# Kernel optimization log

Measured on AMD Instinct MI355X. Metric: run time of the kernel, lower is better.

Reference implementation:

```python
import jax, jax.numpy as jnp
import numpy as np

N, E, G, L = 50000, 800000, 256, 3
D, NF, EF, OUT = 300, 128, 16, 128
BN_EPS = 1e-5


def setup_inputs() -> dict:
    key = jax.random.key(0)
    ks = jax.random.split(key, 24)
    s = 0.02
    inp = {
        "node_feat": jax.random.normal(ks[0], (N, NF), jnp.float32),
        "edge_feat": jax.random.normal(ks[1], (E, EF), jnp.float32),
        "src": jax.random.randint(ks[2], (E,), 0, N),
        "dst": jax.random.randint(ks[3], (E,), 0, N),
        "graph_ids": jnp.sort(jax.random.randint(ks[4], (N,), 0, G)),
        "num_graphs": G,
        # encoder params
        "node_W": jax.random.normal(ks[5], (NF, D), jnp.float32) * s,
        "node_b": jnp.zeros((D,), jnp.float32),
        # per-layer edge encoders [L, EF, D]
        "edge_W": jax.random.normal(ks[6], (L, EF, D), jnp.float32) * s,
        "edge_b": jnp.zeros((L, D), jnp.float32),
        # per-layer GINEConv MLP: Linear(D,2D) BN ReLU Linear(2D,D) BN
        "W1": jax.random.normal(ks[7], (L, D, 2 * D), jnp.float32) * s,
        "b1": jnp.zeros((L, 2 * D), jnp.float32),
        "g1": jnp.ones((L, 2 * D), jnp.float32),
        "beta1": jnp.zeros((L, 2 * D), jnp.float32),
        "W2": jax.random.normal(ks[8], (L, 2 * D, D), jnp.float32) * s,
        "b2": jnp.zeros((L, D), jnp.float32),
        "g2": jnp.ones((L, D), jnp.float32),
        "beta2": jnp.zeros((L, D), jnp.float32),
        # prediction head
        "pred_W": jax.random.normal(ks[9], (D, OUT), jnp.float32) * s,
        "pred_b": jnp.zeros((OUT,), jnp.float32),
    }
    return inp


def _bn(x, g, b):
    # BatchNorm1d in training mode: biased batch statistics
    m = jnp.mean(x, axis=0)
    v = jnp.var(x, axis=0)
    return (x - m) * jax.lax.rsqrt(v + BN_EPS) * g + b


def reference(node_feat, edge_feat, src, dst, graph_ids, num_graphs,
              node_W, node_b, edge_W, edge_b,
              W1, b1, g1, beta1, W2, b2, g2, beta2,
              pred_W, pred_b):
    n_nodes = node_feat.shape[0]
    n_layers = edge_W.shape[0]
    hn = node_feat @ node_W + node_b  # [N, D]
    for l in range(n_layers):
        he = edge_feat @ edge_W[l] + edge_b[l]            # [E, D]
        msg = jax.nn.relu(hn[src] + he)                   # gather + edge fuse
        agg = jax.ops.segment_sum(msg, dst, num_segments=n_nodes)
        h = hn + agg                                      # (1+eps)*h + agg, eps=0
        h = jax.nn.relu(_bn(h @ W1[l] + b1[l], g1[l], beta1[l]))
        h = _bn(h @ W2[l] + b2[l], g2[l], beta2[l])
        hn = jax.nn.relu(h) if l != n_layers - 1 else h   # dropout p=0 -> identity
    # AvgPooling over nodes per graph
    cnt = jax.ops.segment_sum(jnp.ones((n_nodes, 1), hn.dtype), graph_ids,
                              num_segments=num_graphs)
    hg = jax.ops.segment_sum(hn, graph_ids, num_segments=num_graphs)
    hg = hg / jnp.maximum(cnt, 1.0)
    return hg @ pred_W + pred_b  # [G, OUT]
```

## Files before the change

### kernel.cpp

```cpp
#include <hip/hip_runtime.h>

#define N_NODES 50000
#define N_EDGES 800000
#define N_GRAPHS 256
#define N_LAYERS 3
#define DIM 300
#define NFEAT 128
#define EFEAT 16
#define OUTD 128
#define BN_EPS 1e-5f

typedef __attribute__((ext_vector_type(8))) short bfrag8;
typedef __attribute__((ext_vector_type(4))) float facc4;
typedef __attribute__((ext_vector_type(4))) unsigned short us4;
typedef __attribute__((ext_vector_type(8))) unsigned short us8;

__device__ __forceinline__ unsigned short f2bf(float f) {
    unsigned u = __float_as_uint(f);
    unsigned r = ((u >> 16) & 1u) + 0x7fffu;
    return (unsigned short)((u + r) >> 16);
}
__device__ __forceinline__ float bf2f(unsigned short h) {
    return __uint_as_float(((unsigned)h) << 16);
}
__device__ __forceinline__ void split2(float v, unsigned short& h, unsigned short& l) {
    h = f2bf(v);
    l = f2bf(v - bf2f(h));
}

__device__ __forceinline__ void load_lds16(const void* gsrc, void* ldsdst) {
    __builtin_amdgcn_global_load_lds(
        (const __attribute__((address_space(1))) unsigned int*)gsrc,
        (__attribute__((address_space(3))) unsigned int*)ldsdst,
        16, 0, 0);
}

#define MFMA16(a, b, c) __builtin_amdgcn_mfma_f32_16x16x32_bf16(a, b, c, 0, 0, 0)

__global__ __launch_bounds__(256) void tobf4(
    const float* __restrict__ x, unsigned short* __restrict__ H, int n4)
{
    int i = blockIdx.x * 256 + threadIdx.x;
    if (i >= n4) return;
    float4 v = ((const float4*)x)[i];
    us4 h;
    h.x = f2bf(v.x); h.y = f2bf(v.y); h.z = f2bf(v.z); h.w = f2bf(v.w);
    ((us4*)H)[i] = h;
}

__global__ __launch_bounds__(256) void conv_wt(
    const float* __restrict__ W, unsigned short* __restrict__ H,
    unsigned short* __restrict__ L, int K, int N, int Kp, int Np)
{
    int idx = blockIdx.x * 256 + threadIdx.x;
    if (idx >= Np * Kp) return;
    int n = idx / Kp;
    int k = idx - n * Kp;
    float v = (n < N && k < K) ? W[(size_t)k * N + n] : 0.f;
    unsigned short h, l;
    split2(v, h, l);
    H[idx] = h;
    L[idx] = l;
}

__global__ __launch_bounds__(256, 2) void gemm_pp(
    const unsigned short* __restrict__ Ah,
    const unsigned short* __restrict__ Bth, const unsigned short* __restrict__ Btl,
    const float* __restrict__ bias, float* __restrict__ C,
    int M, int N, int Kp, float* __restrict__ stats)
{
    __shared__ unsigned short lds[12288];
    const int tid = threadIdx.x;
    const int lane = tid & 63;
    const int w = tid >> 6;
    const int m0 = blockIdx.x * 128;
    const int n0 = blockIdx.y * 128;
    const int wm = (w & 1) * 64;
    const int wn = (w >> 1) * 64;

    const int srow = lane >> 2;
    const int scol = (lane & 3) * 8;

    const unsigned short* gp[6];
    unsigned loff[6];
#pragma unroll
    for (int i = 0; i < 6; ++i) {
        int c = w * 6 + i;
        const unsigned short* pl = (c < 8) ? Ah : (c < 16) ? Bth : Btl;
        int rowg;
        if (c < 8) {
            rowg = m0 + (c & 7) * 16 + srow;
            rowg = min(rowg, M - 1);
        } else {
            rowg = n0 + (c & 7) * 16 + srow;
        }
        gp[i] = pl + (size_t)rowg * Kp + scol;
        loff[i] = c * 512;
    }

    facc4 acc[4][4];
    facc4 zero = {0.f, 0.f, 0.f, 0.f};
#pragma unroll
    for (int i = 0; i < 4; ++i)
#pragma unroll
        for (int j = 0; j < 4; ++j) acc[i][j] = zero;

    const int fr = lane & 15;
    const int fq = (lane >> 4) * 8;

    for (int k0 = 0; k0 < Kp; k0 += 32) {
#pragma unroll
        for (int i = 0; i < 6; ++i) {
            load_lds16(gp[i], &lds[loff[i]]);
            gp[i] += 32;
        }
        __syncthreads();

        bfrag8 ah[4], bh[4], bl[4];
#pragma unroll
        for (int t = 0; t < 4; ++t) {
            int ar = wm + t * 16 + fr;
            ah[t] = *(const bfrag8*)&lds[ar * 32 + fq];
            int br = wn + t * 16 + fr;
            bh[t] = *(const bfrag8*)&lds[4096 + br * 32 + fq];
            bl[t] = *(const bfrag8*)&lds[8192 + br * 32 + fq];
        }
#pragma unroll
        for (int i = 0; i < 4; ++i)
#pragma unroll
            for (int j = 0; j < 4; ++j) {
                acc[i][j] = MFMA16(ah[i], bh[j], acc[i][j]);
                acc[i][j] = MFMA16(ah[i], bl[j], acc[i][j]);
            }
        __syncthreads();
    }

#pragma unroll
    for (int i = 0; i < 4; ++i)
#pragma unroll
        for (int j = 0; j < 4; ++j) {
            int col = n0 + wn + j * 16 + (lane & 15);
            if (col >= N) continue;
            float bv = bias[col];
#pragma unroll
            for (int r = 0; r < 4; ++r) {
                int row = m0 + wm + i * 16 + (lane >> 4) * 4 + r;
                if (row < M)
                    C[(size_t)row * N + col] = acc[i][j][r] + bv;
            }
        }

    if (stats != nullptr) {
#pragma unroll
        for (int j = 0; j < 4; ++j) {
            int col = n0 + wn + j * 16 + (lane & 15);
            float cs = 0.f, cq = 0.f;
            if (col < N) {
                float bv = bias[col];
#pragma unroll
                for (int i = 0; i < 4; ++i)
#pragma unroll
                    for (int r = 0; r < 4; ++r) {
                        int row = m0 + wm + i * 16 + (lane >> 4) * 4 + r;
                        if (row < M) {
                            float y = acc[i][j][r] + bv;
                            cs += y;
                            cq = fmaf(y, y, cq);
                        }
                    }
            }
            cs += __shfl_xor(cs, 16, 64); cq += __shfl_xor(cq, 16, 64);
            cs += __shfl_xor(cs, 32, 64); cq += __shfl_xor(cq, 32, 64);
            if ((lane >> 4) == 0 && col < N) {
                atomicAdd(&stats[col], cs);
                atomicAdd(&stats[N + col], cq);
            }
        }
    }
}

__global__ __launch_bounds__(256, 2) void gemm_af(
    const float* __restrict__ A, const unsigned short* __restrict__ Bth,
    const unsigned short* __restrict__ Btl, const float* __restrict__ bias,
    float* __restrict__ C, int M, int N, int K, int Kp,
    const float* __restrict__ abn, float* __restrict__ stats)
{
    __shared__ unsigned short lds[12288];
    const int tid = threadIdx.x;
    const int lane = tid & 63;
    const int w = tid >> 6;
    const int m0 = blockIdx.x * 128;
    const int n0 = blockIdx.y * 128;
    const int wm = (w & 1) * 64;
    const int wn = (w >> 1) * 64;

    const int srow = lane >> 2;
    const int scol = (lane & 3) * 8;

    const unsigned short* gpb[4];
    unsigned loffb[4];
#pragma unroll
    for (int i = 0; i < 4; ++i) {
        int c = w * 4 + i;
        const unsigned short* pl = (c < 8) ? Bth : Btl;
        int rowg = n0 + (c & 7) * 16 + srow;
        gpb[i] = pl + (size_t)rowg * Kp + scol;
        loffb[i] = 4096 + c * 512;
    }

    facc4 acc[4][4];
    facc4 zero = {0.f, 0.f, 0.f, 0.f};
#pragma unroll
    for (int i = 0; i < 4; ++i)
#pragma unroll
        for (int j = 0; j < 4; ++j) acc[i][j] = zero;

    const int fr = lane & 15;
    const int fq = (lane >> 4) * 8;

    for (int k0 = 0; k0 < Kp; k0 += 32) {
#pragma unroll
        for (int i = 0; i < 4; ++i) {
            load_lds16(gpb[i], &lds[loffb[i]]);
            gpb[i] += 32;
        }
#pragma unroll
        for (int i = 0; i < 4; ++i) {
            int idx = tid + i * 256;
            int row = idx >> 3;
            int q4 = idx & 7;
            int rg = min(m0 + row, M - 1);
            int kk = k0 + q4 * 4;
            us4 h;
            if (kk < K) {
                float4 v = *(const float4*)&A[(size_t)rg * K + kk];
                float4 sa = *(const float4*)&abn[kk];
                float4 sb = *(const float4*)&abn[K + kk];
                h.x = f2bf(fmaxf(fmaf(v.x, sa.x, sb.x), 0.f));
                h.y = f2bf(fmaxf(fmaf(v.y, sa.y, sb.y), 0.f));
                h.z = f2bf(fmaxf(fmaf(v.z, sa.z, sb.z), 0.f));
                h.w = f2bf(fmaxf(fmaf(v.w, sa.w, sb.w), 0.f));
            } else {
                h.x = 0; h.y = 0; h.z = 0; h.w = 0;
            }
            *(us4*)&lds[row * 32 + q4 * 4] = h;
        }
        __syncthreads();

        bfrag8 ah[4], bh[4], bl[4];
#pragma unroll
        for (int t = 0; t < 4; ++t) {
            int ar = wm + t * 16 + fr;
            ah[t] = *(const bfrag8*)&lds[ar * 32 + fq];
            int br = wn + t * 16 + fr;
            bh[t] = *(const bfrag8*)&lds[4096 + br * 32 + fq];
            bl[t] = *(const bfrag8*)&lds[8192 + br * 32 + fq];
        }
#pragma unroll
        for (int i = 0; i < 4; ++i)
#pragma unroll
            for (int j = 0; j < 4; ++j) {
                acc[i][j] = MFMA16(ah[i], bh[j], acc[i][j]);
                acc[i][j] = MFMA16(ah[i], bl[j], acc[i][j]);
            }
        __syncthreads();
    }

#pragma unroll
    for (int i = 0; i < 4; ++i)
#pragma unroll
        for (int j = 0; j < 4; ++j) {
            int col = n0 + wn + j * 16 + (lane & 15);
            if (col >= N) continue;
            float bv = bias[col];
#pragma unroll
            for (int r = 0; r < 4; ++r) {
                int row = m0 + wm + i * 16 + (lane >> 4) * 4 + r;
                if (row < M)
                    C[(size_t)row * N + col] = acc[i][j][r] + bv;
            }
        }

    if (stats != nullptr) {
#pragma unroll
        for (int j = 0; j < 4; ++j) {
            int col = n0 + wn + j * 16 + (lane & 15);
            float cs = 0.f, cq = 0.f;
            if (col < N) {
                float bv = bias[col];
#pragma unroll
                for (int i = 0; i < 4; ++i)
#pragma unroll
                    for (int r = 0; r < 4; ++r) {
                        int row = m0 + wm + i * 16 + (lane >> 4) * 4 + r;
                        if (row < M) {
                            float y = acc[i][j][r] + bv;
                            cs += y;
                            cq = fmaf(y, y, cq);
                        }
                    }
            }
            cs += __shfl_xor(cs, 16, 64); cq += __shfl_xor(cq, 16, 64);
            cs += __shfl_xor(cs, 32, 64); cq += __shfl_xor(cq, 32, 64);
            if ((lane >> 4) == 0 && col < N) {
                atomicAdd(&stats[col], cs);
                atomicAdd(&stats[N + col], cq);
            }
        }
    }
}

__global__ __launch_bounds__(256) void csr_count(const int* __restrict__ dst, int* __restrict__ P)
{
    int e = blockIdx.x * 256 + threadIdx.x;
    if (e < N_EDGES) atomicAdd(&P[dst[e] + 1], 1);
}

__global__ __launch_bounds__(1024) void csr_scan(int* __restrict__ P)
{
    __shared__ int part[1024];
    const int t = threadIdx.x;
    const int CH = 49;
    int i0 = t * CH;
    int s = 0;
    for (int i = i0; i < i0 + CH; ++i) {
        if (i <= N_NODES) { s += P[i]; P[i] = s; }
    }
    part[t] = s;
    __syncthreads();
    if (t == 0) {
        int run = 0;
        for (int k = 0; k < 1024; ++k) { int tmp = part[k]; part[k] = run; run += tmp; }
    }
    __syncthreads();
    int off = part[t];
    for (int i = i0; i < i0 + CH; ++i) {
        if (i <= N_NODES) P[i] += off;
    }
}

__global__ __launch_bounds__(256) void csr_fill(
    const int* __restrict__ dst, int* __restrict__ P, int* __restrict__ eids)
{
    int e = blockIdx.x * 256 + threadIdx.x;
    if (e < N_EDGES) {
        int pos = atomicAdd(&P[dst[e]], 1);
        eids[pos] = e;
    }
}

__global__ __launch_bounds__(256) void edge_pack_bf(
    const int* __restrict__ src, const int* __restrict__ eids,
    const float* __restrict__ edge_feat, int* __restrict__ es,
    unsigned short* __restrict__ efsb)
{
    int j = blockIdx.x * 256 + threadIdx.x;
    if (j >= N_EDGES) return;
    int e = eids[j];
    es[j] = src[e];
    const float* sp = edge_feat + (size_t)e * EFEAT;
    us8 o0, o1;
#pragma unroll
    for (int k = 0; k < 8; ++k) {
        o0[k] = f2bf(sp[k]);
        o1[k] = f2bf(sp[8 + k]);
    }
    *(us8*)&efsb[(size_t)j * EFEAT] = o0;
    *(us8*)&efsb[(size_t)j * EFEAT + 8] = o1;
}

__global__ __launch_bounds__(256) void gather_agg7(
    const float* __restrict__ hn, const unsigned short* __restrict__ efsb,
    const int* __restrict__ es, const int* __restrict__ P,
    const float* __restrict__ eW, const float* __restrict__ eb,
    unsigned short* __restrict__ aggH)
{
    const int v = blockIdx.x * 4 + (threadIdx.x >> 6);
    if (v >= N_NODES) return;
    const int lane = threadIdx.x & 63;

    float wr[EFEAT][5];
    float acc[5];
    float ebv[5];
#pragma unroll
    for (int c = 0; c < 5; ++c) {
        int d = lane + 64 * c;
        bool dv = d < DIM;
        acc[c] = dv ? hn[(size_t)v * DIM + d] : 0.f;
        ebv[c] = dv ? eb[d] : 0.f;
#pragma unroll
        for (int k = 0; k < EFEAT; ++k)
            wr[k][c] = dv ? eW[k * DIM + d] : 0.f;
    }

    const int j0 = (v == 0) ? 0 : P[v - 1];
    const int j1 = P[v];

    int j = j0;
    for (; j + 4 <= j1; j += 4) {
        int s0 = __builtin_amdgcn_readfirstlane(es[j]);
        int s1 = __builtin_amdgcn_readfirstlane(es[j + 1]);
        int s2 = __builtin_amdgcn_readfirstlane(es[j + 2]);
        int s3 = __builtin_amdgcn_readfirstlane(es[j + 3]);
        const float* __restrict__ h0 = hn + (size_t)s0 * DIM;
        const float* __restrict__ h1 = hn + (size_t)s1 * DIM;
        const float* __restrict__ h2p = hn + (size_t)s2 * DIM;
        const float* __restrict__ h3 = hn + (size_t)s3 * DIM;
        float hv[4][5];
#pragma unroll
        for (int c = 0; c < 5; ++c) {
            int d = lane + 64 * c;
            bool dv = d < DIM;
            hv[0][c] = dv ? h0[d] : 0.f;
            hv[1][c] = dv ? h1[d] : 0.f;
            hv[2][c] = dv ? h2p[d] : 0.f;
            hv[3][c] = dv ? h3[d] : 0.f;
        }
        us8 pk[4][2];
#pragma unroll
        for (int u = 0; u < 4; ++u) {
            pk[u][0] = *(const us8*)&efsb[(size_t)(j + u) * EFEAT];
            pk[u][1] = *(const us8*)&efsb[(size_t)(j + u) * EFEAT + 8];
        }
#pragma unroll
        for (int u = 0; u < 4; ++u) {
            float ef[EFEAT];
#pragma unroll
            for (int k = 0; k < 8; ++k) {
                ef[k] = bf2f(pk[u][0][k]);
                ef[8 + k] = bf2f(pk[u][1][k]);
            }
#pragma unroll
            for (int c = 0; c < 5; ++c) {
                float he = ebv[c];
#pragma unroll
                for (int k = 0; k < EFEAT; ++k) he = fmaf(ef[k], wr[k][c], he);
                acc[c] += fmaxf(hv[u][c] + he, 0.f);
            }
        }
    }
    for (; j < j1; ++j) {
        int s = __builtin_amdgcn_readfirstlane(es[j]);
        const float* __restrict__ hp = hn + (size_t)s * DIM;
        float hv[5];
#pragma unroll
        for (int c = 0; c < 5; ++c) {
            int d = lane + 64 * c;
            hv[c] = (d < DIM) ? hp[d] : 0.f;
        }
        us8 p0 = *(const us8*)&efsb[(size_t)j * EFEAT];
        us8 p1 = *(const us8*)&efsb[(size_t)j * EFEAT + 8];
        float ef[EFEAT];
#pragma unroll
        for (int k = 0; k < 8; ++k) {
            ef[k] = bf2f(p0[k]);
            ef[8 + k] = bf2f(p1[k]);
        }
#pragma unroll
        for (int c = 0; c < 5; ++c) {
            float he = ebv[c];
#pragma unroll
            for (int k = 0; k < EFEAT; ++k) he = fmaf(ef[k], wr[k][c], he);
            acc[c] += fmaxf(hv[c] + he, 0.f);
        }
    }

#pragma unroll
    for (int c = 0; c < 5; ++c)
        aggH[(size_t)v * 320 + lane + 64 * c] = f2bf(acc[c]);
}

__global__ __launch_bounds__(256) void bn_finalize(
    const float* __restrict__ stats, const float* __restrict__ g,
    const float* __restrict__ beta, float* __restrict__ ab, int C)
{
    int c = blockIdx.x * 256 + threadIdx.x;
    if (c >= C) return;
    const float invN = 1.f / (float)N_NODES;
    float m = stats[c] * invN;
    float v = stats[C + c] * invN - m * m;
    float a = g[c] * rsqrtf(v + BN_EPS);
    ab[c] = a;
    ab[C + c] = beta[c] - m * a;
}

__global__ __launch_bounds__(256) void bn_apply(
    const float* __restrict__ x, const float* __restrict__ ab,
    float* __restrict__ y, int total4, int C, int relu)
{
    int i = blockIdx.x * 256 + threadIdx.x;
    if (i >= total4) return;
    float4 v = ((const float4*)x)[i];
    int c = (i << 2) % C;
    const float* a = ab + c;
    const float* bb = ab + C + c;
    float4 r;
    r.x = fmaf(v.x, a[0], bb[0]);
    r.y = fmaf(v.y, a[1], bb[1]);
    r.z = fmaf(v.z, a[2], bb[2]);
    r.w = fmaf(v.w, a[3], bb[3]);
    if (relu) {
        r.x = fmaxf(r.x, 0.f); r.y = fmaxf(r.y, 0.f);
        r.z = fmaxf(r.z, 0.f); r.w = fmaxf(r.w, 0.f);
    }
    ((float4*)y)[i] = r;
}

__global__ __launch_bounds__(256) void pool_seg_bn(
    const float* __restrict__ h2, const int* __restrict__ gid,
    const float* __restrict__ ab, float* __restrict__ hg)
{
    const int g = blockIdx.x;
    int lo = 0, hi = N_NODES;
    while (lo < hi) { int mid = (lo + hi) >> 1; if (gid[mid] < g) lo = mid + 1; else hi = mid; }
    int lo2 = lo, hi2 = N_NODES;
    while (lo2 < hi2) { int mid = (lo2 + hi2) >> 1; if (gid[mid] < g + 1) lo2 = mid + 1; else hi2 = mid; }
    const float inv = 1.f / fmaxf((float)(lo2 - lo), 1.f);
    for (int d = threadIdx.x; d < DIM; d += 256) {
        float s = 0.f;
        for (int r = lo; r < lo2; ++r) s += h2[(size_t)r * DIM + d];
        hg[(size_t)g * DIM + d] = fmaf(s * inv, ab[d], ab[DIM + d]);
    }
}

#define TS 64
#define BK 16
#define ASP 68

__global__ __launch_bounds__(256) void sgemm_bias(
    const float* __restrict__ A, const float* __restrict__ B,
    const float* __restrict__ bias, float* __restrict__ C,
    int M, int Ncol, int K)
{
    __shared__ float As[BK][ASP];
    __shared__ float Bs[BK][TS];
    const int tid = threadIdx.x;
    const int bm = blockIdx.x * TS;
    const int bn = blockIdx.y * TS;
    const int tm = (tid >> 4) * 4;
    const int tn = (tid & 15) * 4;
    float acc[4][4] = {};

    for (int k0 = 0; k0 < K; k0 += BK) {
#pragma unroll
        for (int i = 0; i < 4; ++i) {
            int idx = tid + i * 256;
            int m = idx >> 4;
            int k = idx & 15;
            int row = bm + m, kk = k0 + k;
            float v = 0.f;
            if (row < M && kk < K) v = A[(size_t)row * K + kk];
            As[k][m] = v;
        }
#pragma unroll
        for (int i = 0; i < 4; ++i) {
            int idx = tid + i * 256;
            int k = idx >> 6;
            int n = idx & 63;
            int col = bn + n, kk = k0 + k;
            float v = 0.f;
            if (col < Ncol && kk < K) v = B[(size_t)kk * Ncol + col];
            Bs[k][n] = v;
        }
        __syncthreads();
#pragma unroll
        for (int k = 0; k < BK; ++k) {
            float4 av = *(const float4*)&As[k][tm];
            float4 bv = *(const float4*)&Bs[k][tn];
            float a4[4] = {av.x, av.y, av.z, av.w};
            float b4[4] = {bv.x, bv.y, bv.z, bv.w};
#pragma unroll
            for (int i = 0; i < 4; ++i)
#pragma unroll
                for (int j = 0; j < 4; ++j)
                    acc[i][j] = fmaf(a4[i], b4[j], acc[i][j]);
        }
        __syncthreads();
    }

#pragma unroll
    for (int i = 0; i < 4; ++i) {
        int row = bm + tm + i;
        if (row >= M) continue;
#pragma unroll
        for (int j = 0; j < 4; ++j) {
            int col = bn + tn + j;
            if (col < Ncol)
                C[(size_t)row * Ncol + col] = acc[i][j] + bias[col];
        }
    }
}

extern "C" void kernel_launch(void* const* d_in, const int* in_sizes, int n_in,
                              void* d_out, int out_size, void* d_ws, size_t ws_size,
                              hipStream_t stream)
{
    const float* node_feat = (const float*)d_in[0];
    const float* edge_feat = (const float*)d_in[1];
    const int*   src       = (const int*)d_in[2];
    const int*   dst       = (const int*)d_in[3];
    const int*   gid       = (const int*)d_in[4];
    const float* node_W = (const float*)d_in[6];
    const float* node_b = (const float*)d_in[7];
    const float* edge_W = (const float*)d_in[8];
    const float* edge_b = (const float*)d_in[9];
    const float* W1  = (const float*)d_in[10];
    const float* b1  = (const float*)d_in[11];
    const float* g1  = (const float*)d_in[12];
    const float* be1 = (const float*)d_in[13];
    const float* W2  = (const float*)d_in[14];
    const float* b2  = (const float*)d_in[15];
    const float* g2  = (const float*)d_in[16];
    const float* be2 = (const float*)d_in[17];
    const float* pred_W = (const float*)d_in[18];
    const float* pred_b = (const float*)d_in[19];
    float* out = (float*)d_out;

    char* base = (char*)d_ws;
    float* hn            = (float*)(base + 0);
    float* h2            = hn;
    float* x1            = (float*)(base + 60000000);
    unsigned short* nfH  = (unsigned short*)x1;
    unsigned short* aggH = (unsigned short*)(base + 180000000);
    int*   es            = (int*)(base + 212000000);
    unsigned short* efsb = (unsigned short*)(base + 215200000);
    unsigned short* wtH  = (unsigned short*)(base + 244000000);
    unsigned short* wtL  = (unsigned short*)(base + 244500000);
    int*   eids          = (int*)(base + 245000000);
    int*   P             = (int*)(base + 248200000);
    float* stats         = (float*)(base + 248400016);
    float* ab            = (float*)(base + 248407216);
    float* hg            = (float*)(base + 248414416);
    float* stats2        = stats + 1200;
    float* ab2           = ab + 1200;

    dim3 blk(256);

    tobf4<<<dim3((N_NODES * NFEAT / 4 + 255) / 256), blk, 0, stream>>>(
        node_feat, nfH, N_NODES * NFEAT / 4);
    conv_wt<<<dim3((384 * 128 + 255) / 256), blk, 0, stream>>>(
        node_W, wtH, wtL, NFEAT, DIM, 128, 384);
    gemm_pp<<<dim3(391, 3), blk, 0, stream>>>(
        nfH, wtH, wtL, node_b, hn, N_NODES, DIM, 128, nullptr);

    hipMemsetAsync(P, 0, (N_NODES + 1) * sizeof(int), stream);
    csr_count<<<dim3((N_EDGES + 255) / 256), blk, 0, stream>>>(dst, P);
    csr_scan<<<dim3(1), dim3(1024), 0, stream>>>(P);
    csr_fill<<<dim3((N_EDGES + 255) / 256), blk, 0, stream>>>(dst, P, eids);
    edge_pack_bf<<<dim3((N_EDGES + 255) / 256), blk, 0, stream>>>(
        src, eids, edge_feat, es, efsb);

    for (int l = 0; l < N_LAYERS; ++l) {
        gather_agg7<<<dim3((N_NODES + 3) / 4), blk, 0, stream>>>(
            hn, efsb, es, P,
            edge_W + (size_t)l * EFEAT * DIM, edge_b + (size_t)l * DIM, aggH);

        hipMemsetAsync(stats, 0, 1800 * sizeof(float), stream);

        conv_wt<<<dim3((640 * 320 + 255) / 256), blk, 0, stream>>>(
            W1 + (size_t)l * DIM * 2 * DIM, wtH, wtL, DIM, 2 * DIM, 320, 640);
        gemm_pp<<<dim3(391, 5), blk, 0, stream>>>(
            aggH, wtH, wtL, b1 + (size_t)l * 2 * DIM, x1,
            N_NODES, 2 * DIM, 320, stats);
        bn_finalize<<<dim3(3), blk, 0, stream>>>(
            stats, g1 + (size_t)l * 2 * DIM, be1 + (size_t)l * 2 * DIM, ab, 2 * DIM);

        conv_wt<<<dim3((384 * 608 + 255) / 256), blk, 0, stream>>>(
            W2 + (size_t)l * 2 * DIM * DIM, wtH, wtL, 2 * DIM, DIM, 608, 384);
        gemm_af<<<dim3(391, 3), blk, 0, stream>>>(
            x1, wtH, wtL, b2 + (size_t)l * DIM, h2, N_NODES, DIM, 2 * DIM, 608,
            ab, stats2);
        bn_finalize<<<dim3(2), blk, 0, stream>>>(
            stats2, g2 + (size_t)l * DIM, be2 + (size_t)l * DIM, ab2, DIM);

        if (l < N_LAYERS - 1)
            bn_apply<<<dim3((N_NODES * DIM / 4 + 255) / 256), blk, 0, stream>>>(
                h2, ab2, hn, N_NODES * DIM / 4, DIM, 1);
    }

    pool_seg_bn<<<dim3(N_GRAPHS), blk, 0, stream>>>(h2, gid, ab2, hg);
    sgemm_bias<<<dim3((N_GRAPHS + 63) / 64, (OUTD + 63) / 64), blk, 0, stream>>>(
        hg, pred_W, pred_b, out, N_GRAPHS, OUTD, DIM);
}
```

Measured before the change: 2.199 ms.

## Store layer-1 activations in bf16, pad node rows to 320, pack gather math

```diff
diff --git a/kernel.cpp b/kernel.cpp
--- a/kernel.cpp
+++ b/kernel.cpp
@@ -5,6 +5,7 @@
 #define N_GRAPHS 256
 #define N_LAYERS 3
 #define DIM 300
+#define HSTR 320
 #define NFEAT 128
 #define EFEAT 16
 #define OUTD 128
@@ -14,6 +15,7 @@
 typedef __attribute__((ext_vector_type(4))) float facc4;
 typedef __attribute__((ext_vector_type(4))) unsigned short us4;
 typedef __attribute__((ext_vector_type(8))) unsigned short us8;
+typedef __attribute__((ext_vector_type(2))) float f32x2;
 
 __device__ __forceinline__ unsigned short f2bf(float f) {
     unsigned u = __float_as_uint(f);
@@ -66,7 +68,8 @@
 __global__ __launch_bounds__(256, 2) void gemm_pp(
     const unsigned short* __restrict__ Ah,
     const unsigned short* __restrict__ Bth, const unsigned short* __restrict__ Btl,
-    const float* __restrict__ bias, float* __restrict__ C,
+    const float* __restrict__ bias, float* __restrict__ C, int ldc,
+    unsigned short* __restrict__ Cb, int ldcb,
     int M, int N, int Kp, float* __restrict__ stats)
 {
     __shared__ unsigned short lds[12288];
@@ -145,8 +148,11 @@
 #pragma unroll
             for (int r = 0; r < 4; ++r) {
                 int row = m0 + wm + i * 16 + (lane >> 4) * 4 + r;
-                if (row < M)
-                    C[(size_t)row * N + col] = acc[i][j][r] + bv;
+                if (row < M) {
+                    float y = acc[i][j][r] + bv;
+                    if (C != nullptr) C[(size_t)row * ldc + col] = y;
+                    else Cb[(size_t)row * ldcb + col] = f2bf(y);
+                }
             }
         }
 
@@ -180,9 +186,10 @@
 }
 
 __global__ __launch_bounds__(256, 2) void gemm_af(
-    const float* __restrict__ A, const unsigned short* __restrict__ Bth,
-    const unsigned short* __restrict__ Btl, const float* __restrict__ bias,
-    float* __restrict__ C, int M, int N, int K, int Kp,
+    const unsigned short* __restrict__ A, int lda,
+    const unsigned short* __restrict__ Bth, const unsigned short* __restrict__ Btl,
+    const float* __restrict__ bias, float* __restrict__ C, int ldc,
+    int M, int N, int K, int Kp,
     const float* __restrict__ abn, float* __restrict__ stats)
 {
     __shared__ unsigned short lds[12288];
@@ -233,13 +240,13 @@
             int kk = k0 + q4 * 4;
             us4 h;
             if (kk < K) {
-                float4 v = *(const float4*)&A[(size_t)rg * K + kk];
+                us4 xb = *(const us4*)&A[(size_t)rg * lda + kk];
                 float4 sa = *(const float4*)&abn[kk];
                 float4 sb = *(const float4*)&abn[K + kk];
-                h.x = f2bf(fmaxf(fmaf(v.x, sa.x, sb.x), 0.f));
-                h.y = f2bf(fmaxf(fmaf(v.y, sa.y, sb.y), 0.f));
-                h.z = f2bf(fmaxf(fmaf(v.z, sa.z, sb.z), 0.f));
-                h.w = f2bf(fmaxf(fmaf(v.w, sa.w, sb.w), 0.f));
+                h.x = f2bf(fmaxf(fmaf(bf2f(xb.x), sa.x, sb.x), 0.f));
+                h.y = f2bf(fmaxf(fmaf(bf2f(xb.y), sa.y, sb.y), 0.f));
+                h.z = f2bf(fmaxf(fmaf(bf2f(xb.z), sa.z, sb.z), 0.f));
+                h.w = f2bf(fmaxf(fmaf(bf2f(xb.w), sa.w, sb.w), 0.f));
             } else {
                 h.x = 0; h.y = 0; h.z = 0; h.w = 0;
             }
@@ -277,7 +284,7 @@
             for (int r = 0; r < 4; ++r) {
                 int row = m0 + wm + i * 16 + (lane >> 4) * 4 + r;
                 if (row < M)
-                    C[(size_t)row * N + col] = acc[i][j][r] + bv;
+                    C[(size_t)row * ldc + col] = acc[i][j][r] + bv;
             }
         }
 
@@ -369,7 +376,26 @@
     *(us8*)&efsb[(size_t)j * EFEAT + 8] = o1;
 }
 
-__global__ __launch_bounds__(256) void gather_agg7(
+__device__ __forceinline__ void he_edge(
+    const unsigned short* __restrict__ efsb, long j,
+    const f32x2 wr01[EFEAT], const f32x2 wr23[EFEAT], const float wr4[EFEAT],
+    f32x2 eb01, f32x2 eb23, float eb4,
+    f32x2& he01, f32x2& he23, float& he4)
+{
+    us8 p0 = *(const us8*)&efsb[j * EFEAT];
+    us8 p1 = *(const us8*)&efsb[j * EFEAT + 8];
+    he01 = eb01; he23 = eb23; he4 = eb4;
+#pragma unroll
+    for (int k = 0; k < EFEAT; ++k) {
+        float e = bf2f(k < 8 ? p0[k] : p1[k - 8]);
+        f32x2 e2 = {e, e};
+        he01 = __builtin_elementwise_fma(e2, wr01[k], he01);
+        he23 = __builtin_elementwise_fma(e2, wr23[k], he23);
+        he4 = fmaf(e, wr4[k], he4);
+    }
+}
+
+__global__ __launch_bounds__(256) void gather_agg8(
     const float* __restrict__ hn, const unsigned short* __restrict__ efsb,
     const int* __restrict__ es, const int* __restrict__ P,
     const float* __restrict__ eW, const float* __restrict__ eb,
@@ -378,23 +404,31 @@
     const int v = blockIdx.x * 4 + (threadIdx.x >> 6);
     if (v >= N_NODES) return;
     const int lane = threadIdx.x & 63;
-
-    float wr[EFEAT][5];
-    float acc[5];
-    float ebv[5];
-#pragma unroll
-    for (int c = 0; c < 5; ++c) {
-        int d = lane + 64 * c;
-        bool dv = d < DIM;
-        acc[c] = dv ? hn[(size_t)v * DIM + d] : 0.f;
-        ebv[c] = dv ? eb[d] : 0.f;
-#pragma unroll
-        for (int k = 0; k < EFEAT; ++k)
-            wr[k][c] = dv ? eW[k * DIM + d] : 0.f;
-    }
+    const int d4 = lane + 256;
+    const bool dv4 = d4 < DIM;
+
+    f32x2 wr01[EFEAT], wr23[EFEAT];
+    float wr4[EFEAT];
+#pragma unroll
+    for (int k = 0; k < EFEAT; ++k) {
+        wr01[k].x = eW[k * DIM + lane];
+        wr01[k].y = eW[k * DIM + lane + 64];
+        wr23[k].x = eW[k * DIM + lane + 128];
+        wr23[k].y = eW[k * DIM + lane + 192];
+        wr4[k] = dv4 ? eW[k * DIM + d4] : 0.f;
+    }
+    f32x2 eb01 = {eb[lane], eb[lane + 64]};
+    f32x2 eb23 = {eb[lane + 128], eb[lane + 192]};
+    float eb4 = dv4 ? eb[d4] : 0.f;
+
+    const float* __restrict__ hv = hn + (size_t)v * HSTR;
+    f32x2 acc01 = {hv[lane], hv[lane + 64]};
+    f32x2 acc23 = {hv[lane + 128], hv[lane + 192]};
+    float acc4 = hv[d4];
 
     const int j0 = (v == 0) ? 0 : P[v - 1];
     const int j1 = P[v];
+    const f32x2 z2 = {0.f, 0.f};
 
     int j = j0;
     for (; j + 4 <= j1; j += 4) {
@@ -402,72 +436,47 @@
         int s1 = __builtin_amdgcn_readfirstlane(es[j + 1]);
         int s2 = __builtin_amdgcn_readfirstlane(es[j + 2]);
         int s3 = __builtin_amdgcn_readfirstlane(es[j + 3]);
-        const float* __restrict__ h0 = hn + (size_t)s0 * DIM;
-        const float* __restrict__ h1 = hn + (size_t)s1 * DIM;
-        const float* __restrict__ h2p = hn + (size_t)s2 * DIM;
-        const float* __restrict__ h3 = hn + (size_t)s3 * DIM;
-        float hv[4][5];
-#pragma unroll
-        for (int c = 0; c < 5; ++c) {
-            int d = lane + 64 * c;
-            bool dv = d < DIM;
-            hv[0][c] = dv ? h0[d] : 0.f;
-            hv[1][c] = dv ? h1[d] : 0.f;
-            hv[2][c] = dv ? h2p[d] : 0.f;
-            hv[3][c] = dv ? h3[d] : 0.f;
-        }
-        us8 pk[4][2];
+        const float* __restrict__ h0 = hn + (size_t)s0 * HSTR;
+        const float* __restrict__ h1 = hn + (size_t)s1 * HSTR;
+        const float* __restrict__ h2p = hn + (size_t)s2 * HSTR;
+        const float* __restrict__ h3 = hn + (size_t)s3 * HSTR;
+        f32x2 hva[4], hvb[4];
+        float hvc[4];
+        const float* __restrict__ hp[4] = {h0, h1, h2p, h3};
 #pragma unroll
         for (int u = 0; u < 4; ++u) {
-            pk[u][0] = *(const us8*)&efsb[(size_t)(j + u) * EFEAT];
-            pk[u][1] = *(const us8*)&efsb[(size_t)(j + u) * EFEAT + 8];
+            hva[u].x = hp[u][lane];       hva[u].y = hp[u][lane + 64];
+            hvb[u].x = hp[u][lane + 128]; hvb[u].y = hp[u][lane + 192];
+            hvc[u] = hp[u][d4];
         }
 #pragma unroll
         for (int u = 0; u < 4; ++u) {
-            float ef[EFEAT];
-#pragma unroll
-            for (int k = 0; k < 8; ++k) {
-                ef[k] = bf2f(pk[u][0][k]);
-                ef[8 + k] = bf2f(pk[u][1][k]);
-            }
-#pragma unroll
-            for (int c = 0; c < 5; ++c) {
-                float he = ebv[c];
-#pragma unroll
-                for (int k = 0; k < EFEAT; ++k) he = fmaf(ef[k], wr[k][c], he);
-                acc[c] += fmaxf(hv[u][c] + he, 0.f);
-            }
+            f32x2 he01, he23; float he4;
+            he_edge(efsb, j + u, wr01, wr23, wr4, eb01, eb23, eb4, he01, he23, he4);
+            acc01 += __builtin_elementwise_max(hva[u] + he01, z2);
+            acc23 += __builtin_elementwise_max(hvb[u] + he23, z2);
+            acc4 += fmaxf(hvc[u] + he4, 0.f);
         }
     }
     for (; j < j1; ++j) {
         int s = __builtin_amdgcn_readfirstlane(es[j]);
-        const float* __restrict__ hp = hn + (size_t)s * DIM;
-        float hv[5];
-#pragma unroll
-        for (int c = 0; c < 5; ++c) {
-            int d = lane + 64 * c;
-            hv[c] = (d < DIM) ? hp[d] : 0.f;
-        }
-        us8 p0 = *(const us8*)&efsb[(size_t)j * EFEAT];
-        us8 p1 = *(const us8*)&efsb[(size_t)j * EFEAT + 8];
-        float ef[EFEAT];
-#pragma unroll
-        for (int k = 0; k < 8; ++k) {
-            ef[k] = bf2f(p0[k]);
-            ef[8 + k] = bf2f(p1[k]);
-        }
-#pragma unroll
-        for (int c = 0; c < 5; ++c) {
-            float he = ebv[c];
-#pragma unroll
-            for (int k = 0; k < EFEAT; ++k) he = fmaf(ef[k], wr[k][c], he);
-            acc[c] += fmaxf(hv[c] + he, 0.f);
-        }
-    }
-
-#pragma unroll
-    for (int c = 0; c < 5; ++c)
-        aggH[(size_t)v * 320 + lane + 64 * c] = f2bf(acc[c]);
+        const float* __restrict__ hp = hn + (size_t)s * HSTR;
+        f32x2 ha = {hp[lane], hp[lane + 64]};
+        f32x2 hb = {hp[lane + 128], hp[lane + 192]};
+        float hc = hp[d4];
+        f32x2 he01, he23; float he4;
+        he_edge(efsb, j, wr01, wr23, wr4, eb01, eb23, eb4, he01, he23, he4);
+        acc01 += __builtin_elementwise_max(ha + he01, z2);
+        acc23 += __builtin_elementwise_max(hb + he23, z2);
+        acc4 += fmaxf(hc + he4, 0.f);
+    }
+
+    unsigned short* __restrict__ op = aggH + (size_t)v * HSTR;
+    op[lane] = f2bf(acc01.x);
+    op[lane + 64] = f2bf(acc01.y);
+    op[lane + 128] = f2bf(acc23.x);
+    op[lane + 192] = f2bf(acc23.y);
+    op[d4] = dv4 ? f2bf(acc4) : (unsigned short)0;
 }
 
 __global__ __launch_bounds__(256) void bn_finalize(
@@ -484,16 +493,18 @@
     ab[C + c] = beta[c] - m * a;
 }
 
-__global__ __launch_bounds__(256) void bn_apply(
+__global__ __launch_bounds__(256) void bn_apply_s(
     const float* __restrict__ x, const float* __restrict__ ab,
-    float* __restrict__ y, int total4, int C, int relu)
+    float* __restrict__ y, int relu)
 {
     int i = blockIdx.x * 256 + threadIdx.x;
-    if (i >= total4) return;
-    float4 v = ((const float4*)x)[i];
-    int c = (i << 2) % C;
+    if (i >= N_NODES * 75) return;
+    int n = i / 75;
+    int c = (i - n * 75) * 4;
+    size_t o = (size_t)n * (HSTR / 4) + (c >> 2);
+    float4 v = ((const float4*)x)[o];
     const float* a = ab + c;
-    const float* bb = ab + C + c;
+    const float* bb = ab + DIM + c;
     float4 r;
     r.x = fmaf(v.x, a[0], bb[0]);
     r.y = fmaf(v.y, a[1], bb[1]);
@@ -503,7 +514,7 @@
         r.x = fmaxf(r.x, 0.f); r.y = fmaxf(r.y, 0.f);
         r.z = fmaxf(r.z, 0.f); r.w = fmaxf(r.w, 0.f);
     }
-    ((float4*)y)[i] = r;
+    ((float4*)y)[o] = r;
 }
 
 __global__ __launch_bounds__(256) void pool_seg_bn(
@@ -518,7 +529,7 @@
     const float inv = 1.f / fmaxf((float)(lo2 - lo), 1.f);
     for (int d = threadIdx.x; d < DIM; d += 256) {
         float s = 0.f;
-        for (int r = lo; r < lo2; ++r) s += h2[(size_t)r * DIM + d];
+        for (int r = lo; r < lo2; ++r) s += h2[(size_t)r * HSTR + d];
         hg[(size_t)g * DIM + d] = fmaf(s * inv, ab[d], ab[DIM + d]);
     }
 }
@@ -619,29 +630,31 @@
     char* base = (char*)d_ws;
     float* hn            = (float*)(base + 0);
     float* h2            = hn;
-    float* x1            = (float*)(base + 60000000);
-    unsigned short* nfH  = (unsigned short*)x1;
-    unsigned short* aggH = (unsigned short*)(base + 180000000);
-    int*   es            = (int*)(base + 212000000);
-    unsigned short* efsb = (unsigned short*)(base + 215200000);
-    unsigned short* wtH  = (unsigned short*)(base + 244000000);
-    unsigned short* wtL  = (unsigned short*)(base + 244500000);
-    int*   eids          = (int*)(base + 245000000);
-    int*   P             = (int*)(base + 248200000);
-    float* stats         = (float*)(base + 248400016);
-    float* ab            = (float*)(base + 248407216);
-    float* hg            = (float*)(base + 248414416);
+    unsigned short* x1b  = (unsigned short*)(base + 64000000);
+    unsigned short* nfH  = (unsigned short*)x1b;
+    int*   eids          = (int*)(base + 80000000);
+    unsigned short* aggH = (unsigned short*)(base + 124000000);
+    int*   es            = (int*)(base + 156000000);
+    unsigned short* efsb = (unsigned short*)(base + 159200000);
+    unsigned short* wtH  = (unsigned short*)(base + 184800000);
+    unsigned short* wtL  = (unsigned short*)(base + 185800000);
+    int*   P             = (int*)(base + 186800000);
+    float* stats         = (float*)(base + 187000016);
+    float* ab            = (float*)(base + 187007216);
+    float* hg            = (float*)(base + 187014416);
     float* stats2        = stats + 1200;
     float* ab2           = ab + 1200;
 
     dim3 blk(256);
+
+    hipMemsetAsync(hn, 0, (size_t)N_NODES * HSTR * sizeof(float), stream);
 
     tobf4<<<dim3((N_NODES * NFEAT / 4 + 255) / 256), blk, 0, stream>>>(
         node_feat, nfH, N_NODES * NFEAT / 4);
     conv_wt<<<dim3((384 * 128 + 255) / 256), blk, 0, stream>>>(
         node_W, wtH, wtL, NFEAT, DIM, 128, 384);
     gemm_pp<<<dim3(391, 3), blk, 0, stream>>>(
-        nfH, wtH, wtL, node_b, hn, N_NODES, DIM, 128, nullptr);
+        nfH, wtH, wtL, node_b, hn, HSTR, nullptr, 0, N_NODES, DIM, 128, nullptr);
 
     hipMemsetAsync(P, 0, (N_NODES + 1) * sizeof(int), stream);
     csr_count<<<dim3((N_EDGES + 255) / 256), blk, 0, stream>>>(dst, P);
@@ -651,7 +664,7 @@
         src, eids, edge_feat, es, efsb);
 
     for (int l = 0; l < N_LAYERS; ++l) {
-        gather_agg7<<<dim3((N_NODES + 3) / 4), blk, 0, stream>>>(
+        gather_agg8<<<dim3((N_NODES + 3) / 4), blk, 0, stream>>>(
             hn, efsb, es, P,
             edge_W + (size_t)l * EFEAT * DIM, edge_b + (size_t)l * DIM, aggH);
 
@@ -660,7 +673,7 @@
         conv_wt<<<dim3((640 * 320 + 255) / 256), blk, 0, stream>>>(
             W1 + (size_t)l * DIM * 2 * DIM, wtH, wtL, DIM, 2 * DIM, 320, 640);
         gemm_pp<<<dim3(391, 5), blk, 0, stream>>>(
-            aggH, wtH, wtL, b1 + (size_t)l * 2 * DIM, x1,
+            aggH, wtH, wtL, b1 + (size_t)l * 2 * DIM, nullptr, 0, x1b, 600,
             N_NODES, 2 * DIM, 320, stats);
         bn_finalize<<<dim3(3), blk, 0, stream>>>(
             stats, g1 + (size_t)l * 2 * DIM, be1 + (size_t)l * 2 * DIM, ab, 2 * DIM);
@@ -668,14 +681,14 @@
         conv_wt<<<dim3((384 * 608 + 255) / 256), blk, 0, stream>>>(
             W2 + (size_t)l * 2 * DIM * DIM, wtH, wtL, 2 * DIM, DIM, 608, 384);
         gemm_af<<<dim3(391, 3), blk, 0, stream>>>(
-            x1, wtH, wtL, b2 + (size_t)l * DIM, h2, N_NODES, DIM, 2 * DIM, 608,
-            ab, stats2);
+            x1b, 600, wtH, wtL, b2 + (size_t)l * DIM, h2, HSTR,
+            N_NODES, DIM, 2 * DIM, 608, ab, stats2);
         bn_finalize<<<dim3(2), blk, 0, stream>>>(
             stats2, g2 + (size_t)l * DIM, be2 + (size_t)l * DIM, ab2, DIM);
 
         if (l < N_LAYERS - 1)
-            bn_apply<<<dim3((N_NODES * DIM / 4 + 255) / 256), blk, 0, stream>>>(
-                h2, ab2, hn, N_NODES * DIM / 4, DIM, 1);
+            bn_apply_s<<<dim3((N_NODES * 75 + 255) / 256), blk, 0, stream>>>(
+                h2, ab2, hn, 1);
     }
 
     pool_seg_bn<<<dim3(N_GRAPHS), blk, 0, stream>>>(h2, gid, ab2, hg);
```

New measurement: 2.434 ms. 1.11x slower.
